# Kernel tuning notes

Measured on AMD Instinct MI355X. Metric: run time of the kernel, lower is better.

The kernel has to match this reference:

```python
import jax, jax.numpy as jnp
import numpy as np
import math

N = 50000
E = 1_600_000
F_IN = 512
F_OUT = 256
TAO = 3.0


def setup_inputs() -> dict:
    key = jax.random.key(0)
    ks = jax.random.split(key, 12)
    stdv = 1.0 / math.sqrt(F_OUT)
    std_att = 1.0 / math.sqrt(F_OUT)
    std_att_vec = 1.0 / math.sqrt(3)
    inp = {
        "inputx": jax.random.normal(ks[0], (N, F_IN), dtype=jnp.float32),
        "adj_row": jax.random.randint(ks[1], (E,), 0, N, dtype=jnp.int32),
        "adj_col": jax.random.randint(ks[2], (E,), 0, N, dtype=jnp.int32),
        "adj_val": jax.random.uniform(ks[3], (E,), dtype=jnp.float32),
        "sadj_row": jax.random.randint(ks[4], (E,), 0, N, dtype=jnp.int32),
        "sadj_col": jax.random.randint(ks[5], (E,), 0, N, dtype=jnp.int32),
        "sadj_val": jax.random.uniform(ks[6], (E,), dtype=jnp.float32),
        "weight_mlp": jax.random.uniform(ks[7], (F_IN, F_OUT), minval=-stdv, maxval=stdv, dtype=jnp.float32),
        "weight_A": jax.random.uniform(ks[8], (F_IN, F_OUT), minval=-stdv, maxval=stdv, dtype=jnp.float32),
        "weight_As": jax.random.uniform(ks[9], (F_IN, F_OUT), minval=-stdv, maxval=stdv, dtype=jnp.float32),
        "att_vec_k": jax.random.uniform(ks[10], (F_OUT, F_OUT), minval=-std_att, maxval=std_att, dtype=jnp.float32),
        "att_vec_v": jax.random.uniform(ks[11], (3, 3), minval=-std_att_vec, maxval=std_att_vec, dtype=jnp.float32),
    }
    return inp


def _spmm(row, col, val, h):
    # sparse [N,N] @ dense [N,F]: gather source rows, scale, scatter-add to dest
    msgs = val[:, None] * h[col]  # [E, F]
    return jax.ops.segment_sum(msgs, row, num_segments=N)


def reference(inputx, adj_row, adj_col, adj_val, sadj_row, sadj_col, sadj_val,
              weight_mlp, weight_A, weight_As, att_vec_k, att_vec_v):
    output_mlp = jax.nn.relu(inputx @ weight_mlp)                     # [N, F]
    output_A = jax.nn.relu(_spmm(adj_row, adj_col, adj_val, inputx @ weight_A))
    output_As = jax.nn.relu(_spmm(sadj_row, sadj_col, sadj_val, inputx @ weight_As))

    output_stru = output_mlp + output_As + output_A
    K = jnp.mean(output_stru @ att_vec_k, axis=0, keepdims=True)      # [1, F]
    logits = jnp.concatenate([output_mlp @ K.T, output_A @ K.T, output_As @ K.T], axis=1)  # [N, 3]
    att = jax.nn.softmax((jax.nn.sigmoid(logits) @ att_vec_v) / TAO, axis=1)
    alpha_mlp, alpha_A, alpha_As = att[:, 0:1], att[:, 1:2], att[:, 2:3]
    emb = alpha_mlp * output_mlp + alpha_A * output_A + alpha_As * output_As
    return emb
```

## Files before the change

### kernel.cpp

```cpp
#include <hip/hip_runtime.h>
#include <hip/hip_bf16.h>

#define N_NODES 50000
#define E_EDGES 1600000
#define FIN 512
#define FOUT 256
#define NCOMB 768
#define TAO_F 3.0f
#define M_PAD 50048
#define N_RPAD 50048
#define NB 196
#define CSTRIDE 16
#define CH 4096
#define NCH 13
#define RPW 8
#define WPG 6256

#define GEMM_WGS 2346
#define GEMM_Q  (GEMM_WGS / 8)
#define GEMM_R  (GEMM_WGS % 8)

typedef __bf16 bf16x8 __attribute__((ext_vector_type(8)));
typedef float  f32x4  __attribute__((ext_vector_type(4)));

static __device__ __forceinline__ unsigned short f2bf(float f) {
    unsigned int u = __float_as_uint(f);
    u += 0x7FFFu + ((u >> 16) & 1u);
    return (unsigned short)(u >> 16);
}
static __device__ __forceinline__ float bf2f(unsigned short h) {
    return __uint_as_float(((unsigned int)h) << 16);
}

__global__ void convert_x_kernel(const float* __restrict__ X, unsigned short* __restrict__ Xb) {
    long long i = ((long long)blockIdx.x * blockDim.x + threadIdx.x) * 4;
    const long long total = (long long)M_PAD * FIN;
    if (i >= total) return;
    const long long valid = (long long)N_NODES * FIN;
    ushort4 o;
    if (i < valid) {
        const float4 v = *reinterpret_cast<const float4*>(X + i);
        o.x = f2bf(v.x); o.y = f2bf(v.y); o.z = f2bf(v.z); o.w = f2bf(v.w);
    } else {
        o.x = o.y = o.z = o.w = 0;
    }
    *reinterpret_cast<ushort4*>(Xb + i) = o;
}

__global__ void convert_w_kernel(const float* __restrict__ Wm, const float* __restrict__ Wa,
                                 const float* __restrict__ Was, unsigned short* __restrict__ Wt) {
    int i = blockIdx.x * blockDim.x + threadIdx.x;
    if (i >= NCOMB * FIN) return;
    int row = i / FIN, k = i % FIN;
    int w = row >> 8, n = row & 255;
    const float* W = (w == 0) ? Wm : (w == 1) ? Wa : Was;
    Wt[i] = f2bf(W[(size_t)k * FOUT + n]);
}

#define BM 128
#define BN 128
#define BK 64

__global__ __launch_bounds__(256) void gemm_kernel(const unsigned short* __restrict__ A,
                                                   const unsigned short* __restrict__ Bt,
                                                   unsigned short* __restrict__ Hm,
                                                   unsigned short* __restrict__ HA,
                                                   unsigned short* __restrict__ HAs,
                                                   float* __restrict__ colsum8) {
    __shared__ unsigned short As[BM * BK];
    __shared__ unsigned short Bs[BN * BK];
    __shared__ float csm[128];
    const int b = blockIdx.x;
    const int xcd = b & 7, ii = b >> 3;
    const int work = (xcd < GEMM_R ? xcd * (GEMM_Q + 1)
                                   : GEMM_R * (GEMM_Q + 1) + (xcd - GEMM_R) * GEMM_Q) + ii;
    const int py = work / 6, px = work - py * 6;
    const int row0 = py * BM, col0 = px * BN;
    const int tid = threadIdx.x;
    const int lane = tid & 63, wave = tid >> 6;
    const int wr = wave >> 1, wc = wave & 1;
    if (tid < 128) csm[tid] = 0.f;
    const int st_row = tid >> 3;
    const int st_col = (tid & 7) * 8;
    const int lds_off = wave * 512;
    const unsigned short* Ag = A + (size_t)(row0 + st_row) * FIN + st_col;
    const unsigned short* Bg = Bt + (size_t)(col0 + st_row) * FIN + st_col;
    f32x4 acc[4][4] = {};

    for (int k0 = 0; k0 < FIN; k0 += BK) {
#pragma unroll
        for (int i = 0; i < 4; i++) {
            __builtin_amdgcn_global_load_lds(
                (const __attribute__((address_space(1))) unsigned int*)(Ag + (size_t)i * 32 * FIN + k0),
                (__attribute__((address_space(3))) unsigned int*)&As[i * 2048 + lds_off], 16, 0, 0);
            __builtin_amdgcn_global_load_lds(
                (const __attribute__((address_space(1))) unsigned int*)(Bg + (size_t)i * 32 * FIN + k0),
                (__attribute__((address_space(3))) unsigned int*)&Bs[i * 2048 + lds_off], 16, 0, 0);
        }
        __syncthreads();
#pragma unroll
        for (int kk = 0; kk < 2; kk++) {
            bf16x8 af[4], bfr[4];
            const int ko = kk * 32 + (lane >> 4) * 8;
#pragma unroll
            for (int m = 0; m < 4; m++)
                af[m] = *reinterpret_cast<const bf16x8*>(&As[(wr * 64 + m * 16 + (lane & 15)) * BK + ko]);
#pragma unroll
            for (int n = 0; n < 4; n++)
                bfr[n] = *reinterpret_cast<const bf16x8*>(&Bs[(wc * 64 + n * 16 + (lane & 15)) * BK + ko]);
#pragma unroll
            for (int m = 0; m < 4; m++)
#pragma unroll
                for (int n = 0; n < 4; n++)
                    acc[m][n] = __builtin_amdgcn_mfma_f32_16x16x32_bf16(af[m], bfr[n], acc[m][n], 0, 0, 0);
        }
        __syncthreads();
    }

    const int seg = col0 >> 8;
    unsigned short* hp = (seg == 0) ? Hm : (seg == 1) ? HA : HAs;
    const int rb = row0 + wr * 64 + ((lane >> 4) << 2);
    const int cb_loc = wc * 64 + (lane & 15);
    const int cbase = col0 - seg * 256 + cb_loc;
    float part[4] = {0.f, 0.f, 0.f, 0.f};
#pragma unroll
    for (int m = 0; m < 4; m++)
#pragma unroll
        for (int n = 0; n < 4; n++)
#pragma unroll
            for (int j = 0; j < 4; j++) {
                int r = rb + m * 16 + j;
                if (r < N_NODES) {
                    float v = acc[m][n][j];
                    if (seg == 0) { v = fmaxf(v, 0.f); part[n] += v; }
                    hp[(size_t)r * FOUT + cbase + n * 16] = f2bf(v);
                }
            }
    if (seg == 0) {
#pragma unroll
        for (int n = 0; n < 4; n++) atomicAdd(&csm[cb_loc + n * 16], part[n]);
        __syncthreads();
        if (tid < 128) atomicAdd(&colsum8[((b & 7) << 8) + col0 + tid], csm[tid]);
    }
}

__global__ __launch_bounds__(256) void hist_kernel(const int* __restrict__ rowA, int* __restrict__ bcntA,
                                                   const int* __restrict__ rowS, int* __restrict__ bcntS) {
    __shared__ int h[2 * NB];
    const int t = threadIdx.x;
    for (int j = t; j < 2 * NB; j += 256) h[j] = 0;
    __syncthreads();
    int i = blockIdx.x * blockDim.x + t;
    const int stride = gridDim.x * blockDim.x;
    for (; i < E_EDGES; i += stride) {
        atomicAdd(&h[rowA[i] >> 8], 1);
        atomicAdd(&h[NB + (rowS[i] >> 8)], 1);
    }
    __syncthreads();
    for (int j = t; j < 2 * NB; j += 256) {
        int v = h[j];
        if (v) {
            if (j < NB) atomicAdd(&bcntA[j * CSTRIDE], v);
            else        atomicAdd(&bcntS[(j - NB) * CSTRIDE], v);
        }
    }
}

__global__ __launch_bounds__(256) void scan196_kernel(const int* __restrict__ bcntA, int* __restrict__ bstartA,
                                                      int* __restrict__ bcurA,
                                                      const int* __restrict__ bcntS, int* __restrict__ bstartS,
                                                      int* __restrict__ bcurS) {
    __shared__ int wsum[4];
    const int t = threadIdx.x, lane = t & 63, w = t >> 6;
    for (int g = 0; g < 2; g++) {
        const int* bcnt = g ? bcntS : bcntA;
        int* bstart = g ? bstartS : bstartA;
        int* bcur = g ? bcurS : bcurA;
        int v = (t < NB) ? bcnt[t * CSTRIDE] : 0;
        int x = v;
#pragma unroll
        for (int off = 1; off < 64; off <<= 1) { int y = __shfl_up(x, off); if (lane >= off) x += y; }
        if (lane == 63) wsum[w] = x;
        __syncthreads();
        int woff = 0;
        for (int i = 0; i < w; i++) woff += wsum[i];
        int ex = woff + x - v;
        if (t < NB) { bstart[t] = ex; bcur[t * CSTRIDE] = ex; }
        if (t == 0) bstart[NB] = E_EDGES;
        __syncthreads();
    }
}

__global__ __launch_bounds__(256) void pass1_kernel(
    const int* __restrict__ rowA, const int* __restrict__ colA, const float* __restrict__ valA,
    int* __restrict__ bcurA, int2* __restrict__ ed1A,
    const int* __restrict__ rowS, const int* __restrict__ colS, const float* __restrict__ valS,
    int* __restrict__ bcurS, int2* __restrict__ ed1S) {
    __shared__ int lcnt[NB];
    __shared__ int gcur[NB];
    const int t = threadIdx.x;
    const int base = blockIdx.x * CH;
    const int n = min(CH, E_EDGES - base);
    for (int g = 0; g < 2; g++) {
        const int* row = g ? rowS : rowA;
        const int* col = g ? colS : colA;
        const float* val = g ? valS : valA;
        int* bcur = g ? bcurS : bcurA;
        int2* ed1 = g ? ed1S : ed1A;
        for (int j = t; j < NB; j += 256) lcnt[j] = 0;
        __syncthreads();
        for (int j = t; j < n; j += 256) atomicAdd(&lcnt[row[base + j] >> 8], 1);
        __syncthreads();
        for (int j = t; j < NB; j += 256) {
            int c = lcnt[j];
            gcur[j] = c ? atomicAdd(&bcur[j * CSTRIDE], c) : 0;
        }
        __syncthreads();
        for (int j = t; j < n; j += 256) {
            int r = row[base + j];
            int b = r >> 8;
            int pos = atomicAdd(&gcur[b], 1);
            ed1[pos] = make_int2(((r & 255) << 16) | col[base + j], __float_as_int(val[base + j]));
        }
        __syncthreads();
    }
}

__global__ __launch_bounds__(256) void pass2_kernel(
    const int* __restrict__ bstartA, const int2* __restrict__ ed1A, int2* __restrict__ ed2A, int* __restrict__ rpA,
    const int* __restrict__ bstartS, const int2* __restrict__ ed1S, int2* __restrict__ ed2S, int* __restrict__ rpS) {
    const int g = (blockIdx.x >= NB) ? 1 : 0;
    const int b = blockIdx.x - g * NB;
    const int* bstart = g ? bstartS : bstartA;
    const int2* ed1 = g ? ed1S : ed1A;
    int2* ed2 = g ? ed2S : ed2A;
    int* rp = g ? rpS : rpA;
    const int s = bstart[b], e = bstart[b + 1];
    const int t = threadIdx.x, lane = t & 63, w = t >> 6;
    __shared__ int rcnt[256 * NCH];
    __shared__ int lcur[256 * NCH];
    __shared__ int wsum[4];
    for (int j = t; j < 256 * NCH; j += 256) rcnt[j] = 0;
    __syncthreads();
    for (int j = s + t; j < e; j += 256) {
        int2 v2 = ed1[j];
        atomicAdd(&rcnt[(v2.x >> 16) * NCH + ((v2.x & 0xFFFF) >> 12)], 1);
    }
    __syncthreads();
    int rsum = 0;
#pragma unroll
    for (int c = 0; c < NCH; c++) rsum += rcnt[t * NCH + c];
    int x = rsum;
#pragma unroll
    for (int off = 1; off < 64; off <<= 1) { int y = __shfl_up(x, off); if (lane >= off) x += y; }
    if (lane == 63) wsum[w] = x;
    __syncthreads();
    int woff = 0;
    for (int i = 0; i < w; i++) woff += wsum[i];
    const int ex = woff + x - rsum;
    const int row = b * 256 + t;
    if (row < N_NODES) rp[row] = s + ex;
    else if (row <= N_RPAD) rp[row] = E_EDGES;
    int off2 = ex;
#pragma unroll
    for (int c = 0; c < NCH; c++) { lcur[t * NCH + c] = off2; off2 += rcnt[t * NCH + c]; }
    __syncthreads();
    for (int j = s + t; j < e; j += 256) {
        int2 v2 = ed1[j];
        int rl = v2.x >> 16, cc = (v2.x & 0xFFFF) >> 12;
        int k = atomicAdd(&lcur[rl * NCH + cc], 1);
        ed2[s + k] = make_int2(v2.x & 0xFFFF, v2.y);
    }
}

__global__ __launch_bounds__(256) void spmm_kernel(
    const int* __restrict__ rpA, const int2* __restrict__ edA,
    const unsigned short* __restrict__ HA, unsigned short* __restrict__ OA,
    const int* __restrict__ rpS, const int2* __restrict__ edS,
    const unsigned short* __restrict__ HS, unsigned short* __restrict__ OS,
    float* __restrict__ colsum8) {
    __shared__ float csum[256];
    const int t = threadIdx.x, wave = t >> 6, lane = t & 63;
    csum[t] = 0.f;
    __syncthreads();
    const int gwave = blockIdx.x * 4 + wave;
    const int g = (gwave >= WPG) ? 1 : 0;
    const int wv = gwave - g * WPG;
    const int* rp = g ? rpS : rpA;
    const int2* ed = g ? edS : edA;
    const unsigned short* H = g ? HS : HA;
    unsigned short* O = g ? OS : OA;
    const int r0 = wv * RPW;
    float cs0 = 0.f, cs1 = 0.f, cs2 = 0.f, cs3 = 0.f;
    int s = rp[r0];
#pragma unroll
    for (int i = 0; i < RPW; i++) {
        const int r = r0 + i;
        const int e = rp[r + 1];
        float a0 = 0.f, a1 = 0.f, a2 = 0.f, a3 = 0.f;
#pragma unroll 4
        for (int j = s; j < e; ++j) {
            const int2 ev = ed[j];
            const float v = __int_as_float(ev.y);
            const uint2 hv = *reinterpret_cast<const uint2*>(H + (((size_t)ev.x) << 8) + lane * 4);
            a0 += v * bf2f((unsigned short)(hv.x & 0xFFFFu));
            a1 += v * bf2f((unsigned short)(hv.x >> 16));
            a2 += v * bf2f((unsigned short)(hv.y & 0xFFFFu));
            a3 += v * bf2f((unsigned short)(hv.y >> 16));
        }
        s = e;
        if (r < N_NODES) {
            a0 = fmaxf(a0, 0.f); a1 = fmaxf(a1, 0.f);
            a2 = fmaxf(a2, 0.f); a3 = fmaxf(a3, 0.f);
            cs0 += a0; cs1 += a1; cs2 += a2; cs3 += a3;
            ushort4 o;
            o.x = f2bf(a0); o.y = f2bf(a1); o.z = f2bf(a2); o.w = f2bf(a3);
            *reinterpret_cast<ushort4*>(O + (((size_t)r) << 8) + lane * 4) = o;
        }
    }
    atomicAdd(&csum[lane * 4 + 0], cs0);
    atomicAdd(&csum[lane * 4 + 1], cs1);
    atomicAdd(&csum[lane * 4 + 2], cs2);
    atomicAdd(&csum[lane * 4 + 3], cs3);
    __syncthreads();
    atomicAdd(&colsum8[((blockIdx.x & 7) << 8) + t], csum[t]);
}

__global__ void kvec_kernel(const float* __restrict__ colsum8, const float* __restrict__ attk,
                            float* __restrict__ Kv) {
    __shared__ float mean_s[FOUT];
    const int t = threadIdx.x;
    float cs = 0.f;
#pragma unroll
    for (int k = 0; k < 8; k++) cs += colsum8[(k << 8) + t];
    mean_s[t] = cs * (1.0f / (float)N_NODES);
    __syncthreads();
    float acc = 0.f;
    for (int i = 0; i < FOUT; i++) acc += mean_s[i] * attk[(size_t)i * FOUT + t];
    Kv[t] = acc;
}

__global__ __launch_bounds__(256) void final_kernel(float* __restrict__ out,
                                                    const unsigned short* __restrict__ Omb,
                                                    const unsigned short* __restrict__ Oa,
                                                    const unsigned short* __restrict__ Oas,
                                                    const float* __restrict__ Kv,
                                                    const float* __restrict__ attv) {
    const int r = blockIdx.x, t = threadIdx.x, lane = t & 63, w = t >> 6;
    __shared__ float red[4][3];
    __shared__ float alpha[3];
    const size_t o = (size_t)r * FOUT + t;
    const float om = bf2f(Omb[o]), oa = bf2f(Oa[o]), oas = bf2f(Oas[o]);
    const float kv = Kv[t];
    float p0 = om * kv, p1 = oa * kv, p2 = oas * kv;
#pragma unroll
    for (int off = 32; off; off >>= 1) {
        p0 += __shfl_down(p0, off);
        p1 += __shfl_down(p1, off);
        p2 += __shfl_down(p2, off);
    }
    if (lane == 0) { red[w][0] = p0; red[w][1] = p1; red[w][2] = p2; }
    __syncthreads();
    if (t == 0) {
        float l0 = red[0][0] + red[1][0] + red[2][0] + red[3][0];
        float l1 = red[0][1] + red[1][1] + red[2][1] + red[3][1];
        float l2 = red[0][2] + red[1][2] + red[2][2] + red[3][2];
        float s0 = 1.f / (1.f + __expf(-l0));
        float s1 = 1.f / (1.f + __expf(-l1));
        float s2 = 1.f / (1.f + __expf(-l2));
        float q0 = (s0 * attv[0] + s1 * attv[3] + s2 * attv[6]) * (1.f / TAO_F);
        float q1 = (s0 * attv[1] + s1 * attv[4] + s2 * attv[7]) * (1.f / TAO_F);
        float q2 = (s0 * attv[2] + s1 * attv[5] + s2 * attv[8]) * (1.f / TAO_F);
        float mx = fmaxf(q0, fmaxf(q1, q2));
        float e0 = __expf(q0 - mx), e1 = __expf(q1 - mx), e2 = __expf(q2 - mx);
        float inv = 1.f / (e0 + e1 + e2);
        alpha[0] = e0 * inv; alpha[1] = e1 * inv; alpha[2] = e2 * inv;
    }
    __syncthreads();
    out[o] = alpha[0] * om + alpha[1] * oa + alpha[2] * oas;
}

extern "C" void kernel_launch(void* const* d_in, const int* in_sizes, int n_in,
                              void* d_out, int out_size, void* d_ws, size_t ws_size,
                              hipStream_t stream) {
    (void)in_sizes; (void)n_in; (void)out_size; (void)ws_size;
    const float* X        = (const float*)d_in[0];
    const int*   adj_row  = (const int*)d_in[1];
    const int*   adj_col  = (const int*)d_in[2];
    const float* adj_val  = (const float*)d_in[3];
    const int*   sadj_row = (const int*)d_in[4];
    const int*   sadj_col = (const int*)d_in[5];
    const float* sadj_val = (const float*)d_in[6];
    const float* W_mlp    = (const float*)d_in[7];
    const float* W_A      = (const float*)d_in[8];
    const float* W_As     = (const float*)d_in[9];
    const float* attk     = (const float*)d_in[10];
    const float* attv     = (const float*)d_in[11];
    float* out = (float*)d_out;

    char* p = (char*)d_ws;
    auto alloc = [&](size_t bytes) -> char* {
        char* q = p; p += (bytes + 255) & ~(size_t)255; return q;
    };
    unsigned short* Xb   = (unsigned short*)alloc((size_t)M_PAD * FIN * 2);
    unsigned short* Wt   = (unsigned short*)alloc((size_t)NCOMB * FIN * 2);
    unsigned short* H_M  = (unsigned short*)alloc((size_t)N_NODES * FOUT * 2);
    unsigned short* H_A  = (unsigned short*)alloc((size_t)N_NODES * FOUT * 2);
    unsigned short* H_As = (unsigned short*)alloc((size_t)N_NODES * FOUT * 2);
    unsigned short* O_A  = (unsigned short*)alloc((size_t)N_NODES * FOUT * 2);
    unsigned short* O_As = (unsigned short*)alloc((size_t)N_NODES * FOUT * 2);
    int2*  ed1A  = (int2*)alloc((size_t)E_EDGES * 8);
    int2*  ed1S  = (int2*)alloc((size_t)E_EDGES * 8);
    int2*  ed2A  = (int2*)alloc((size_t)E_EDGES * 8);
    int2*  ed2S  = (int2*)alloc((size_t)E_EDGES * 8);
    int*   bcntA = (int*)alloc((size_t)NB * CSTRIDE * 4);
    int*   bcntS = (int*)alloc((size_t)NB * CSTRIDE * 4);
    int*   bcurA = (int*)alloc((size_t)NB * CSTRIDE * 4);
    int*   bcurS = (int*)alloc((size_t)NB * CSTRIDE * 4);
    int*   bstartA = (int*)alloc((size_t)(NB + 1) * 4);
    int*   bstartS = (int*)alloc((size_t)(NB + 1) * 4);
    int*   rpA   = (int*)alloc((size_t)(N_RPAD + 1) * 4);
    int*   rpS   = (int*)alloc((size_t)(N_RPAD + 1) * 4);
    float* colsum8 = (float*)alloc(8 * FOUT * 4);
    float* Kv      = (float*)alloc(FOUT * 4);

    hipMemsetAsync(bcntA, 0, (size_t)NB * CSTRIDE * 4, stream);
    hipMemsetAsync(bcntS, 0, (size_t)NB * CSTRIDE * 4, stream);
    hipMemsetAsync(colsum8, 0, 8 * FOUT * 4, stream);

    {
        long long total = (long long)M_PAD * FIN / 4;
        int blocks = (int)((total + 255) / 256);
        convert_x_kernel<<<blocks, 256, 0, stream>>>(X, Xb);
    }
    convert_w_kernel<<<(NCOMB * FIN + 255) / 256, 256, 0, stream>>>(W_mlp, W_A, W_As, Wt);

    hist_kernel<<<512, 256, 0, stream>>>(adj_row, bcntA, sadj_row, bcntS);
    scan196_kernel<<<1, 256, 0, stream>>>(bcntA, bstartA, bcurA, bcntS, bstartS, bcurS);
    pass1_kernel<<<(E_EDGES + CH - 1) / CH, 256, 0, stream>>>(
        adj_row, adj_col, adj_val, bcurA, ed1A,
        sadj_row, sadj_col, sadj_val, bcurS, ed1S);
    pass2_kernel<<<2 * NB, 256, 0, stream>>>(bstartA, ed1A, ed2A, rpA,
                                             bstartS, ed1S, ed2S, rpS);

    gemm_kernel<<<GEMM_WGS, 256, 0, stream>>>(Xb, Wt, H_M, H_A, H_As, colsum8);

    spmm_kernel<<<(2 * WPG) / 4, 256, 0, stream>>>(rpA, ed2A, H_A, O_A,
                                                   rpS, ed2S, H_As, O_As, colsum8);

    kvec_kernel<<<1, 256, 0, stream>>>(colsum8, attk, Kv);
    final_kernel<<<N_NODES, 256, 0, stream>>>(out, H_M, O_A, O_As, Kv, attv);
}
```

Before: 538.8 us.

## Map one SpMM row per wave with XCD-aware graph split and wider colsum striping

The SpMM kernel now gives each wave a single row instead of eight, which raises the number of waves launched and evens out load across rows. Block indices are remapped so that four of the eight XCDs handle the A graph and four handle the As graph, which should keep each H matrix in fewer L2 caches. Column-sum partials are spread over 64 stripes instead of 8 to reduce global atomic contention. The cost is more blocks and more LDS atomics per row, plus a larger reduction in kvec.

```diff
diff --git a/kernel.cpp b/kernel.cpp
--- a/kernel.cpp
+++ b/kernel.cpp
@@ -13,8 +13,7 @@
 #define CSTRIDE 16
 #define CH 4096
 #define NCH 13
-#define RPW 8
-#define WPG 6256
+#define NSTRIPE 64
 
 #define GEMM_WGS 2346
 #define GEMM_Q  (GEMM_WGS / 8)
@@ -66,7 +65,7 @@
                                                    unsigned short* __restrict__ Hm,
                                                    unsigned short* __restrict__ HA,
                                                    unsigned short* __restrict__ HAs,
-                                                   float* __restrict__ colsum8) {
+                                                   float* __restrict__ colsumS) {
     __shared__ unsigned short As[BM * BK];
     __shared__ unsigned short Bs[BN * BK];
     __shared__ float csm[128];
@@ -140,7 +139,7 @@
 #pragma unroll
         for (int n = 0; n < 4; n++) atomicAdd(&csm[cb_loc + n * 16], part[n]);
         __syncthreads();
-        if (tid < 128) atomicAdd(&colsum8[((b & 7) << 8) + col0 + tid], csm[tid]);
+        if (tid < 128) atomicAdd(&colsumS[((b & (NSTRIPE - 1)) << 8) + col0 + tid], csm[tid]);
     }
 }
 
@@ -278,61 +277,54 @@
     const unsigned short* __restrict__ HA, unsigned short* __restrict__ OA,
     const int* __restrict__ rpS, const int2* __restrict__ edS,
     const unsigned short* __restrict__ HS, unsigned short* __restrict__ OS,
-    float* __restrict__ colsum8) {
+    float* __restrict__ colsumS) {
     __shared__ float csum[256];
     const int t = threadIdx.x, wave = t >> 6, lane = t & 63;
     csum[t] = 0.f;
     __syncthreads();
-    const int gwave = blockIdx.x * 4 + wave;
-    const int g = (gwave >= WPG) ? 1 : 0;
-    const int wv = gwave - g * WPG;
+    const int b = blockIdx.x;
+    const int xcd = b & 7;
+    const int g = xcd >> 2;
+    const int lb = (b >> 3) * 4 + (xcd & 3);
+    const int r = lb * 4 + wave;
     const int* rp = g ? rpS : rpA;
     const int2* ed = g ? edS : edA;
     const unsigned short* H = g ? HS : HA;
     unsigned short* O = g ? OS : OA;
-    const int r0 = wv * RPW;
-    float cs0 = 0.f, cs1 = 0.f, cs2 = 0.f, cs3 = 0.f;
-    int s = rp[r0];
-#pragma unroll
-    for (int i = 0; i < RPW; i++) {
-        const int r = r0 + i;
-        const int e = rp[r + 1];
-        float a0 = 0.f, a1 = 0.f, a2 = 0.f, a3 = 0.f;
+    const int s = rp[r], e = rp[r + 1];
+    float a0 = 0.f, a1 = 0.f, a2 = 0.f, a3 = 0.f;
 #pragma unroll 4
-        for (int j = s; j < e; ++j) {
-            const int2 ev = ed[j];
-            const float v = __int_as_float(ev.y);
-            const uint2 hv = *reinterpret_cast<const uint2*>(H + (((size_t)ev.x) << 8) + lane * 4);
-            a0 += v * bf2f((unsigned short)(hv.x & 0xFFFFu));
-            a1 += v * bf2f((unsigned short)(hv.x >> 16));
-            a2 += v * bf2f((unsigned short)(hv.y & 0xFFFFu));
-            a3 += v * bf2f((unsigned short)(hv.y >> 16));
-        }
-        s = e;
-        if (r < N_NODES) {
-            a0 = fmaxf(a0, 0.f); a1 = fmaxf(a1, 0.f);
-            a2 = fmaxf(a2, 0.f); a3 = fmaxf(a3, 0.f);
-            cs0 += a0; cs1 += a1; cs2 += a2; cs3 += a3;
-            ushort4 o;
-            o.x = f2bf(a0); o.y = f2bf(a1); o.z = f2bf(a2); o.w = f2bf(a3);
-            *reinterpret_cast<ushort4*>(O + (((size_t)r) << 8) + lane * 4) = o;
-        }
-    }
-    atomicAdd(&csum[lane * 4 + 0], cs0);
-    atomicAdd(&csum[lane * 4 + 1], cs1);
-    atomicAdd(&csum[lane * 4 + 2], cs2);
-    atomicAdd(&csum[lane * 4 + 3], cs3);
-    __syncthreads();
-    atomicAdd(&colsum8[((blockIdx.x & 7) << 8) + t], csum[t]);
-}
-
-__global__ void kvec_kernel(const float* __restrict__ colsum8, const float* __restrict__ attk,
+    for (int j = s; j < e; ++j) {
+        const int2 ev = ed[j];
+        const float v = __int_as_float(ev.y);
+        const uint2 hv = *reinterpret_cast<const uint2*>(H + (((size_t)ev.x) << 8) + lane * 4);
+        a0 += v * bf2f((unsigned short)(hv.x & 0xFFFFu));
+        a1 += v * bf2f((unsigned short)(hv.x >> 16));
+        a2 += v * bf2f((unsigned short)(hv.y & 0xFFFFu));
+        a3 += v * bf2f((unsigned short)(hv.y >> 16));
+    }
+    if (r < N_NODES) {
+        a0 = fmaxf(a0, 0.f); a1 = fmaxf(a1, 0.f);
+        a2 = fmaxf(a2, 0.f); a3 = fmaxf(a3, 0.f);
+        ushort4 o;
+        o.x = f2bf(a0); o.y = f2bf(a1); o.z = f2bf(a2); o.w = f2bf(a3);
+        *reinterpret_cast<ushort4*>(O + (((size_t)r) << 8) + lane * 4) = o;
+        atomicAdd(&csum[lane * 4 + 0], a0);
+        atomicAdd(&csum[lane * 4 + 1], a1);
+        atomicAdd(&csum[lane * 4 + 2], a2);
+        atomicAdd(&csum[lane * 4 + 3], a3);
+    }
+    __syncthreads();
+    atomicAdd(&colsumS[((b & (NSTRIPE - 1)) << 8) + t], csum[t]);
+}
+
+__global__ void kvec_kernel(const float* __restrict__ colsumS, const float* __restrict__ attk,
                             float* __restrict__ Kv) {
     __shared__ float mean_s[FOUT];
     const int t = threadIdx.x;
     float cs = 0.f;
 #pragma unroll
-    for (int k = 0; k < 8; k++) cs += colsum8[(k << 8) + t];
+    for (int k = 0; k < NSTRIPE; k++) cs += colsumS[(k << 8) + t];
     mean_s[t] = cs * (1.0f / (float)N_NODES);
     __syncthreads();
     float acc = 0.f;
@@ -421,12 +413,12 @@
     int*   bstartS = (int*)alloc((size_t)(NB + 1) * 4);
     int*   rpA   = (int*)alloc((size_t)(N_RPAD + 1) * 4);
     int*   rpS   = (int*)alloc((size_t)(N_RPAD + 1) * 4);
-    float* colsum8 = (float*)alloc(8 * FOUT * 4);
+    float* colsumS = (float*)alloc((size_t)NSTRIPE * FOUT * 4);
     float* Kv      = (float*)alloc(FOUT * 4);
 
     hipMemsetAsync(bcntA, 0, (size_t)NB * CSTRIDE * 4, stream);
     hipMemsetAsync(bcntS, 0, (size_t)NB * CSTRIDE * 4, stream);
-    hipMemsetAsync(colsum8, 0, 8 * FOUT * 4, stream);
+    hipMemsetAsync(colsumS, 0, (size_t)NSTRIPE * FOUT * 4, stream);
 
     {
         long long total = (long long)M_PAD * FIN / 4;
@@ -443,11 +435,11 @@
     pass2_kernel<<<2 * NB, 256, 0, stream>>>(bstartA, ed1A, ed2A, rpA,
                                              bstartS, ed1S, ed2S, rpS);
 
-    gemm_kernel<<<GEMM_WGS, 256, 0, stream>>>(Xb, Wt, H_M, H_A, H_As, colsum8);
-
-    spmm_kernel<<<(2 * WPG) / 4, 256, 0, stream>>>(rpA, ed2A, H_A, O_A,
-                                                   rpS, ed2S, H_As, O_As, colsum8);
-
-    kvec_kernel<<<1, 256, 0, stream>>>(colsum8, attk, Kv);
+    gemm_kernel<<<GEMM_WGS, 256, 0, stream>>>(Xb, Wt, H_M, H_A, H_As, colsumS);
+
+    spmm_kernel<<<(2 * N_RPAD) / 4, 256, 0, stream>>>(rpA, ed2A, H_A, O_A,
+                                                      rpS, ed2S, H_As, O_As, colsumS);
+
+    kvec_kernel<<<1, 256, 0, stream>>>(colsumS, attk, Kv);
     final_kernel<<<N_NODES, 256, 0, stream>>>(out, H_M, O_A, O_As, Kv, attv);
 }
```

New measurement: 560.8 us. +4.1%, slower.
